# Kernel tuning notes

Hardware: AMD Instinct MI355X
Metric: run time of the kernel (lower is better)

## Reference

```python
import jax, jax.numpy as jnp
import numpy as np

D_MODEL = 1024
NUM_HEADS = 16
D_K = D_MODEL // NUM_HEADS
LN_EPS = 1e-5


def setup_inputs() -> dict:
    key = jax.random.key(0)
    ks = jax.random.split(key, 16)
    B, SQ, SK = 2, 2048, 2048
    s = 1.0 / np.sqrt(D_MODEL)
    inp = {
        "query": jax.random.normal(ks[0], (B, SQ, D_MODEL), jnp.float32),
        "key": jax.random.normal(ks[1], (B, SK, D_MODEL), jnp.float32),
        "value": jax.random.normal(ks[2], (B, SK, D_MODEL), jnp.float32),
        "mask": jax.random.randint(ks[3], (B, SQ, SK), 0, 2, jnp.int32),
        "w_q": jax.random.normal(ks[4], (D_MODEL, D_MODEL), jnp.float32) * s,
        "b_q": jnp.zeros((D_MODEL,), jnp.float32),
        "w_k": jax.random.normal(ks[5], (D_MODEL, D_MODEL), jnp.float32) * s,
        "b_k": jnp.zeros((D_MODEL,), jnp.float32),
        "w_v": jax.random.normal(ks[6], (D_MODEL, D_MODEL), jnp.float32) * s,
        "b_v": jnp.zeros((D_MODEL,), jnp.float32),
        "w_o": jax.random.normal(ks[7], (D_MODEL, D_MODEL), jnp.float32) * s,
        "b_o": jnp.zeros((D_MODEL,), jnp.float32),
        "ln_gamma": jnp.ones((D_MODEL,), jnp.float32),
        "ln_beta": jnp.zeros((D_MODEL,), jnp.float32),
    }
    return inp


def _split_heads(x):
    B, S, _ = x.shape
    return x.reshape(B, S, NUM_HEADS, D_K).transpose(0, 2, 1, 3)  # [B,H,S,Dk]


def reference(query, key, value, mask, w_q, b_q, w_k, b_k, w_v, b_v, w_o, b_o, ln_gamma, ln_beta):
    residual = query
    # torch Linear: y = x @ W.T + b
    Q = _split_heads(jnp.einsum('bsd,ed->bse', query, w_q) + b_q)
    K = _split_heads(jnp.einsum('bsd,ed->bse', key, w_k) + b_k)
    V = _split_heads(jnp.einsum('bsd,ed->bse', value, w_v) + b_v)
    scores = jnp.einsum('bhqd,bhkd->bhqk', Q, K) / jnp.sqrt(jnp.float32(D_K))
    scores = jnp.where(mask[:, None, :, :] == 0, jnp.float32(-1e9), scores)
    attn = jax.nn.softmax(scores, axis=-1)
    # dropout: eval mode (identity)
    ctx = jnp.einsum('bhqk,bhkd->bhqd', attn, V)
    B, H, SQ, Dk = ctx.shape
    ctx = ctx.transpose(0, 2, 1, 3).reshape(B, SQ, D_MODEL)
    out = jnp.einsum('bsd,ed->bse', ctx, w_o) + b_o + residual
    mu = jnp.mean(out, axis=-1, keepdims=True)
    var = jnp.mean(jnp.square(out - mu), axis=-1, keepdims=True)
    out = (out - mu) * jax.lax.rsqrt(var + LN_EPS) * ln_gamma + ln_beta
    return out
```

## Files before the change

### kernel.cpp

```cpp
#include <hip/hip_runtime.h>

typedef unsigned short u16;
typedef __attribute__((ext_vector_type(8))) short bf16x8;
typedef __attribute__((ext_vector_type(4))) float f32x4;

#define LOG2E 1.4426950408889634f
#define QSCALE (LOG2E / 8.0f)

__device__ __forceinline__ u16 f2bf(float f) {
  union { float f; unsigned u; } v; v.f = f;
  unsigned r = v.u + 0x7fffu + ((v.u >> 16) & 1u);
  return (u16)(r >> 16);
}

__device__ __forceinline__ float bf2f(u16 u) {
  union { unsigned u; float f; } v; v.u = (unsigned)u << 16; return v.f;
}

__device__ __forceinline__ void gload_lds16(const void* g, void* l) {
  __builtin_amdgcn_global_load_lds(
      (const __attribute__((address_space(1))) unsigned int*)(unsigned long long)g,
      (__attribute__((address_space(3))) unsigned int*)(unsigned int)(unsigned long long)l,
      16, 0, 0);
}

__global__ __launch_bounds__(256) void prep_kernel(
    const float* __restrict__ q, const float* __restrict__ k, const float* __restrict__ v,
    const float* __restrict__ wq, const float* __restrict__ wk, const float* __restrict__ wv,
    const float* __restrict__ wo, const int* __restrict__ mask,
    u16* __restrict__ Xq, u16* __restrict__ Xk, u16* __restrict__ Xv,
    u16* __restrict__ Wq, u16* __restrict__ Wk, u16* __restrict__ Wv, u16* __restrict__ Wo,
    unsigned long long* __restrict__ Mp) {
  const int bx = blockIdx.x;
  if (bx < 16384) {
    const float* src; u16* dst; float sc; int idx;
    if (bx < 12288) {
      int seg = bx >> 12;
      idx = (bx & 4095) * 256 + threadIdx.x;
      src = seg == 0 ? q : (seg == 1 ? k : v);
      dst = seg == 0 ? Xq : (seg == 1 ? Xk : Xv);
      sc = 1.f;
    } else {
      int t = bx - 12288, seg = t >> 10;
      idx = (t & 1023) * 256 + threadIdx.x;
      src = seg == 0 ? wq : (seg == 1 ? wk : (seg == 2 ? wv : wo));
      dst = seg == 0 ? Wq : (seg == 1 ? Wk : (seg == 2 ? Wv : Wo));
      sc = seg == 0 ? QSCALE : 1.f;
    }
    float4 x = ((const float4*)src)[idx];
    ushort4 o;
    o.x = f2bf(x.x * sc); o.y = f2bf(x.y * sc);
    o.z = f2bf(x.z * sc); o.w = f2bf(x.w * sc);
    ((ushort4*)dst)[idx] = o;
  } else {
    int gw = (((bx - 16384) * 256) + threadIdx.x) >> 6;
    int lane = threadIdx.x & 63;
    for (int w = gw; w < 131072; w += 16384) {
      int m = mask[(size_t)w * 64 + lane];
      unsigned long long b = __ballot(m != 0);
      if (lane == 0) Mp[w] = b;
    }
  }
}

__global__ __launch_bounds__(256, 3) void gemm_kernel(
    const u16* __restrict__ Xq, const u16* __restrict__ Xk, const u16* __restrict__ Xv,
    const u16* __restrict__ Wq, const u16* __restrict__ Wk, const u16* __restrict__ Wv,
    const u16* __restrict__ Wo, const u16* __restrict__ Ctx,
    const float* __restrict__ bq, const float* __restrict__ bk, const float* __restrict__ bv,
    u16* __restrict__ Qd, u16* __restrict__ Kd, u16* __restrict__ Vtd, u16* __restrict__ outp,
    int mode_base) {
  __shared__ __align__(16) u16 SH[17408];
  u16* As = SH;
  u16* Bs = SH + 4096;
  const int mode = mode_base + blockIdx.z;
  const int tid = threadIdx.x;
  const int wid = tid >> 6, l = tid & 63, quad = l >> 4, ln = l & 15;
  const int wm = wid >> 1, wn = wid & 1;

  const u16 *A, *B; const float* bias;
  if (mode == 0)      { A = Wq; B = Xq;  bias = bq; }
  else if (mode == 1) { A = Wk; B = Xk;  bias = bk; }
  else if (mode == 2) { A = Xv; B = Wv;  bias = bv; }
  else                { A = Wo; B = Ctx; bias = bq; }
  int mBase, nBase;
  if (mode == 2) { mBase = blockIdx.x * 128; nBase = blockIdx.y * 128; }
  else           { mBase = blockIdx.y * 128; nBase = blockIdx.x * 128; }

  const int koff = (mode >= 3) ? (mode - 3) * 512 : 0;
  const int kLen = (mode >= 3) ? 512 : 1024;
  const u16* Ag = A + (size_t)mBase * 1024 + koff;
  const u16* Bg = B + (size_t)nBase * 1024 + koff;

  f32x4 acc[4][4] = {};

  for (int k0 = 0; k0 < kLen; k0 += 32) {
    if (k0) __syncthreads();
    {
      int i0 = tid, i1 = tid + 256;
      gload_lds16(Ag + (size_t)(i0 & 127) * 1024 + k0 + (i0 >> 7) * 8, &As[i0 * 8]);
      gload_lds16(Ag + (size_t)(i1 & 127) * 1024 + k0 + (i1 >> 7) * 8, &As[i1 * 8]);
      gload_lds16(Bg + (size_t)(i0 & 127) * 1024 + k0 + (i0 >> 7) * 8, &Bs[i0 * 8]);
      gload_lds16(Bg + (size_t)(i1 & 127) * 1024 + k0 + (i1 >> 7) * 8, &Bs[i1 * 8]);
    }
    __syncthreads();
    bf16x8 af[4], bf[4];
#pragma unroll
    for (int i = 0; i < 4; ++i)
      af[i] = *(const bf16x8*)&As[(quad * 128 + wm * 64 + i * 16 + ln) * 8];
#pragma unroll
    for (int j = 0; j < 4; ++j)
      bf[j] = *(const bf16x8*)&Bs[(quad * 128 + wn * 64 + j * 16 + ln) * 8];
#pragma unroll
    for (int i = 0; i < 4; ++i)
#pragma unroll
      for (int j = 0; j < 4; ++j)
        acc[i][j] = __builtin_amdgcn_mfma_f32_16x16x32_bf16(af[i], bf[j], acc[i][j], 0, 0, 0);
  }

  __syncthreads();

  if (mode <= 1) {
    const float bscale = (mode == 0) ? QSCALE : 1.0f;
#pragma unroll
    for (int i = 0; i < 4; ++i) {
      int f0 = wm * 64 + i * 16 + quad * 4;
      float4 bb = *(const float4*)(bias + mBase + f0);
#pragma unroll
      for (int j = 0; j < 4; ++j) {
        int sl = wn * 64 + j * 16 + ln;
        f32x4 v = acc[i][j];
        ushort4 o;
        o.x = f2bf(v[0] + bb.x * bscale); o.y = f2bf(v[1] + bb.y * bscale);
        o.z = f2bf(v[2] + bb.z * bscale); o.w = f2bf(v[3] + bb.w * bscale);
        *(ushort4*)&SH[sl * 136 + f0] = o;
      }
    }
    __syncthreads();
    u16* dstQK = (mode == 0) ? Qd : Kd;
#pragma unroll
    for (int p = 0; p < 8; ++p) {
      int sl = p * 16 + (tid >> 4);
      int fl = (tid & 15) * 8;
      uint4 w = *(const uint4*)&SH[sl * 136 + fl];
      int s = nBase + sl, f = mBase + fl;
      int h = f >> 6, d = f & 63, b = s >> 11, sr = s & 2047;
      *(uint4*)(dstQK + (((size_t)(b * 16 + h) * 2048 + sr) * 64 + d)) = w;
    }
  } else if (mode == 2) {
#pragma unroll
    for (int j = 0; j < 4; ++j) {
      int fl = wn * 64 + j * 16 + ln;
      float bb = bias[nBase + fl];
#pragma unroll
      for (int i = 0; i < 4; ++i) {
        int s0 = wm * 64 + i * 16 + quad * 4;
        f32x4 v = acc[i][j];
        ushort4 o;
        o.x = f2bf(v[0] + bb); o.y = f2bf(v[1] + bb);
        o.z = f2bf(v[2] + bb); o.w = f2bf(v[3] + bb);
        *(ushort4*)&SH[fl * 136 + s0] = o;
      }
    }
    __syncthreads();
#pragma unroll
    for (int p = 0; p < 8; ++p) {
      int fl = p * 16 + (tid >> 4);
      int sl = (tid & 15) * 8;
      uint4 w = *(const uint4*)&SH[fl * 136 + sl];
      int f = nBase + fl, s = mBase + sl;
      int h = f >> 6, d = f & 63, b = s >> 11, sr = s & 2047;
      *(uint4*)(Vtd + (((size_t)(b * 16 + h) * 64 + d) * 2048 + sr)) = w;
    }
  } else {
    u16* dst = outp + (size_t)(mode - 3) * (4096u * 1024u);
#pragma unroll
    for (int i = 0; i < 4; ++i) {
      int f0 = wm * 64 + i * 16 + quad * 4;
#pragma unroll
      for (int j = 0; j < 4; ++j) {
        int sl = wn * 64 + j * 16 + ln;
        f32x4 v = acc[i][j];
        ushort4 o;
        o.x = f2bf(v[0]); o.y = f2bf(v[1]);
        o.z = f2bf(v[2]); o.w = f2bf(v[3]);
        *(ushort4*)&SH[sl * 136 + f0] = o;
      }
    }
    __syncthreads();
#pragma unroll
    for (int p = 0; p < 8; ++p) {
      int sl = p * 16 + (tid >> 4);
      int fl = (tid & 15) * 8;
      uint4 w = *(const uint4*)&SH[sl * 136 + fl];
      *(uint4*)(dst + (size_t)(nBase + sl) * 1024 + mBase + fl) = w;
    }
  }
}

__global__ __launch_bounds__(512, 4) void attn_kernel(
    const u16* __restrict__ Qg, const u16* __restrict__ Kg, const u16* __restrict__ Vtg,
    const unsigned* __restrict__ Mp, u16* __restrict__ ctx) {
  __shared__ __align__(16) u16 Ks0[8192];
  __shared__ __align__(16) u16 Ks1[8192];
  __shared__ __align__(16) u16 Vs0[8192];
  __shared__ __align__(16) u16 Vs1[8192];
  __shared__ __align__(16) u16 Ps[8192];
  const int tid = threadIdx.x;
  const int wid = tid >> 6, l = tid & 63, quad = l >> 4, ln = l & 15;
  const int q4 = quad * 4;
  const int L = blockIdx.x;
  const int bh = (L & 7) + 8 * (L >> 7);
  const int b = bh >> 4, h = bh & 15;
  const int qBase = ((L >> 3) & 15) * 128;
  const int wq = wid * 16;
  const int sw = (ln & 7) << 3;

  bf16x8 qf[2];
#pragma unroll
  for (int kc = 0; kc < 2; ++kc)
    qf[kc] = *(const bf16x8*)(Qg + (((size_t)bh * 2048 + qBase + wq + ln) * 64 +
                                    kc * 32 + quad * 8));

  f32x4 oacc[4] = {};
  f32x4 lsum = {};
  const bf16x8 vone = {(short)0x3F80, (short)0x3F80, (short)0x3F80, (short)0x3F80,
                       (short)0x3F80, (short)0x3F80, (short)0x3F80, (short)0x3F80};

  const unsigned* mrow = Mp + ((size_t)b * 2048 + qBase + wq + ln) * 64;

  const u16* KgB = Kg + (size_t)bh * 2048 * 64;
  const u16* VgB = Vtg + (size_t)bh * 64 * 2048;

#define STAGE_TILE(KS, VS, t_)                                                  \
  do {                                                                          \
    const int kvB_ = (t_) * 128;                                                \
    _Pragma("unroll")                                                           \
    for (int r_ = 0; r_ < 2; ++r_) {                                            \
      int c_ = r_ * 512 + tid;                                                  \
      gload_lds16(KgB + (size_t)(kvB_ + (c_ & 127)) * 64 + (c_ >> 7) * 8,       \
                  &KS[c_ * 8]);                                                 \
      gload_lds16(VgB + (size_t)(c_ & 63) * 2048 + kvB_ + (c_ >> 6) * 8,        \
                  &VS[c_ * 8]);                                                 \
    }                                                                           \
  } while (0)

#define COMPUTE_TILE(KS, VS, it_)                                                         \
  do {                                                                                    \
    unsigned ww[4];                                                                       \
    {                                                                                     \
      uint4 m0 = *(const uint4*)(mrow + (it_) * 4);                                       \
      ww[0] = m0.x; ww[1] = m0.y; ww[2] = m0.z; ww[3] = m0.w;                             \
    }                                                                                     \
    _Pragma("unroll")                                                                     \
    for (int hf = 0; hf < 2; ++hf) {                                                      \
      f32x4 s[4];                                                                         \
      __builtin_amdgcn_s_setprio(1);                                                      \
      _Pragma("unroll")                                                                   \
      for (int m2 = 0; m2 < 4; ++m2) {                                                    \
        int mt = hf * 4 + m2;                                                             \
        bf16x8 k0 = *(const bf16x8*)&KS[((0 + quad) * 128 + mt * 16 + ln) * 8];           \
        bf16x8 k1 = *(const bf16x8*)&KS[((4 + quad) * 128 + mt * 16 + ln) * 8];           \
        f32x4 z = {0.f, 0.f, 0.f, 0.f};                                                   \
        z = __builtin_amdgcn_mfma_f32_16x16x32_bf16(k0, qf[0], z, 0, 0, 0);               \
        s[m2] = __builtin_amdgcn_mfma_f32_16x16x32_bf16(k1, qf[1], z, 0, 0, 0);           \
      }                                                                                   \
      __builtin_amdgcn_s_setprio(0);                                                      \
      uint2 pk[4];                                                                        \
      _Pragma("unroll")                                                                   \
      for (int m2 = 0; m2 < 4; ++m2) {                                                    \
        int mt = hf * 4 + m2;                                                             \
        unsigned nib = (ww[mt >> 1] >> ((mt & 1) * 16 + q4)) & 0xFu;                      \
        float p0 = __builtin_amdgcn_exp2f((nib & 1u) ? s[m2][0] : -1e30f);                \
        float p1 = __builtin_amdgcn_exp2f((nib & 2u) ? s[m2][1] : -1e30f);                \
        float p2 = __builtin_amdgcn_exp2f((nib & 4u) ? s[m2][2] : -1e30f);                \
        float p3 = __builtin_amdgcn_exp2f((nib & 8u) ? s[m2][3] : -1e30f);                \
        pk[m2].x = __builtin_amdgcn_perm(__float_as_uint(p1), __float_as_uint(p0),        \
                                         0x07060302u);                                    \
        pk[m2].y = __builtin_amdgcn_perm(__float_as_uint(p3), __float_as_uint(p2),        \
                                         0x07060302u);                                    \
      }                                                                                   \
              \
      _Pragma("unroll")                                                                   \
      for (int m2 = 0; m2 < 4; ++m2)                                                      \
        *(uint2*)&Ps[(((wq + ln) * 64) + m2 * 16 + q4) ^ sw] = pk[m2];                    \
      __builtin_amdgcn_s_setprio(1);                                                      \
      _Pragma("unroll")                                                                   \
      for (int k2 = 0; k2 < 2; ++k2) {                                                    \
        int kc2 = hf * 2 + k2;                                                            \
        bf16x8 aP = *(const bf16x8*)&Ps[(((wq + ln) * 64) + k2 * 32 + quad * 8) ^ sw];    \
        _Pragma("unroll")                                                                 \
        for (int nt = 0; nt < 4; ++nt) {                                                  \
          bf16x8 bV = *(const bf16x8*)&VS[((kc2 * 4 + quad) * 64 + nt * 16 + ln) * 8];    \
          oacc[nt] = __builtin_amdgcn_mfma_f32_16x16x32_bf16(aP, bV, oacc[nt], 0, 0, 0);  \
        }                                                                                 \
        lsum = __builtin_amdgcn_mfma_f32_16x16x32_bf16(aP, vone, lsum, 0, 0, 0);          \
      }                                                                                   \
      __builtin_amdgcn_s_setprio(0);                                                      \
    }                                                                                     \
  } while (0)

  STAGE_TILE(Ks0, Vs0, 0);
#pragma unroll 1
  for (int it2 = 0; it2 < 8; ++it2) {
    __syncthreads();
    STAGE_TILE(Ks1, Vs1, 2 * it2 + 1);
    COMPUTE_TILE(Ks0, Vs0, 2 * it2);
    __syncthreads();
    if (it2 < 7) STAGE_TILE(Ks0, Vs0, 2 * it2 + 2);
    COMPUTE_TILE(Ks1, Vs1, 2 * it2 + 1);
  }
#undef STAGE_TILE
#undef COMPUTE_TILE

  __syncthreads();
#pragma unroll
  for (int r = 0; r < 4; ++r) {
    float il = 1.0f / lsum[r];
    int q = wq + q4 + r;
#pragma unroll
    for (int nt = 0; nt < 4; ++nt)
      Ps[q * 64 + nt * 16 + ln] = f2bf(oacc[nt][r] * il);
  }
  __syncthreads();
#pragma unroll
  for (int r = 0; r < 2; ++r) {
    int c = r * 512 + tid;
    int q = c >> 3, ch = c & 7;
    *(uint4*)(ctx + ((size_t)(b * 2048 + qBase + q) * 1024 + h * 64 + ch * 8)) =
        *(const uint4*)&Ps[q * 64 + ch * 8];
  }
}

__global__ __launch_bounds__(256) void ln_kernel(const u16* __restrict__ xp,
                                                 const float* __restrict__ resid,
                                                 const float* __restrict__ bo,
                                                 const float* __restrict__ gamma,
                                                 const float* __restrict__ beta,
                                                 float* __restrict__ out) {
  __shared__ float red[8];
  const int tid = threadIdx.x;
  const size_t row = blockIdx.x;
  ushort4 pa = ((const ushort4*)(xp + row * 1024))[tid];
  ushort4 pb = ((const ushort4*)(xp + 4096u * 1024u + row * 1024))[tid];
  const float4 rr = ((const float4*)(resid + row * 1024))[tid];
  const float4 bb = ((const float4*)bo)[tid];
  float4 v;
  v.x = bf2f(pa.x) + bf2f(pb.x) + rr.x + bb.x;
  v.y = bf2f(pa.y) + bf2f(pb.y) + rr.y + bb.y;
  v.z = bf2f(pa.z) + bf2f(pb.z) + rr.z + bb.z;
  v.w = bf2f(pa.w) + bf2f(pb.w) + rr.w + bb.w;
  float s1 = v.x + v.y + v.z + v.w;
  float s2 = v.x * v.x + v.y * v.y + v.z * v.z + v.w * v.w;
#pragma unroll
  for (int o = 32; o >= 1; o >>= 1) {
    s1 += __shfl_xor(s1, o);
    s2 += __shfl_xor(s2, o);
  }
  if ((tid & 63) == 0) { red[(tid >> 6) * 2] = s1; red[(tid >> 6) * 2 + 1] = s2; }
  __syncthreads();
  s1 = red[0] + red[2] + red[4] + red[6];
  s2 = red[1] + red[3] + red[5] + red[7];
  float mu = s1 * (1.f / 1024.f);
  float var = s2 * (1.f / 1024.f) - mu * mu;
  float inv = rsqrtf(var + 1e-5f);
  float4 g = ((const float4*)gamma)[tid];
  float4 be = ((const float4*)beta)[tid];
  float4 o;
  o.x = (v.x - mu) * inv * g.x + be.x;
  o.y = (v.y - mu) * inv * g.y + be.y;
  o.z = (v.z - mu) * inv * g.z + be.z;
  o.w = (v.w - mu) * inv * g.w + be.w;
  ((float4*)(out + row * 1024))[tid] = o;
}

extern "C" void kernel_launch(void* const* d_in, const int* in_sizes, int n_in,
                              void* d_out, int out_size, void* d_ws, size_t ws_size,
                              hipStream_t stream) {
  const float* query = (const float*)d_in[0];
  const float* key   = (const float*)d_in[1];
  const float* value = (const float*)d_in[2];
  const int*   mask  = (const int*)d_in[3];
  const float* w_q = (const float*)d_in[4];
  const float* b_q = (const float*)d_in[5];
  const float* w_k = (const float*)d_in[6];
  const float* b_k = (const float*)d_in[7];
  const float* w_v = (const float*)d_in[8];
  const float* b_v = (const float*)d_in[9];
  const float* w_o = (const float*)d_in[10];
  const float* b_o = (const float*)d_in[11];
  const float* ln_g = (const float*)d_in[12];
  const float* ln_b = (const float*)d_in[13];
  float* out = (float*)d_out;

  char* ws = (char*)d_ws;
  u16* Xq = (u16*)(ws + ((size_t)0 << 20));
  u16* Xk = (u16*)(ws + ((size_t)8 << 20));
  u16* Xv = (u16*)(ws + ((size_t)16 << 20));
  u16* outpre = (u16*)(ws + ((size_t)8 << 20));
  u16* Wq = (u16*)(ws + ((size_t)24 << 20));
  u16* Wk = (u16*)(ws + ((size_t)26 << 20));
  u16* Wv = (u16*)(ws + ((size_t)28 << 20));
  u16* Wo = (u16*)(ws + ((size_t)30 << 20));
  u16* Qd = (u16*)(ws + ((size_t)32 << 20));
  u16* Kd = (u16*)(ws + ((size_t)40 << 20));
  u16* Vtd = (u16*)(ws + ((size_t)48 << 20));
  unsigned long long* Mp = (unsigned long long*)(ws + ((size_t)56 << 20));
  u16* ctx = Xq;

  prep_kernel<<<20480, 256, 0, stream>>>(query, key, value, w_q, w_k, w_v, w_o, mask,
                                         Xq, Xk, Xv, Wq, Wk, Wv, Wo, Mp);
  gemm_kernel<<<dim3(32, 8, 3), 256, 0, stream>>>(Xq, Xk, Xv, Wq, Wk, Wv, Wo, ctx,
      b_q, b_k, b_v, Qd, Kd, Vtd, outpre, 0);
  attn_kernel<<<dim3(512), 512, 0, stream>>>(Qd, Kd, Vtd, (const unsigned*)Mp, ctx);
  gemm_kernel<<<dim3(32, 8, 2), 256, 0, stream>>>(Xq, Xk, Xv, Wq, Wk, Wv, Wo, ctx,
      b_q, b_k, b_v, Qd, Kd, Vtd, outpre, 3);
  ln_kernel<<<4096, 256, 0, stream>>>(outpre, query, b_o, ln_g, ln_b, out);
}
```

Measured before the change: 297.1 us.

## Split attention KV tile across 4 wave groups with 1024-thread blocks and LDS reduction

The attention kernel moves from 512 to 1024 threads per block. Each wave now handles 32 query rows against a quarter of every 128-key tile, rather than 16 rows against the whole tile. Partial output and row-sum accumulators from the four key groups are reduced serially through shared memory at the end. The aim is more waves in flight to hide latency and more reuse of K/V fragments across two query tiles. In exchange it adds a serialized reduction with extra syncs, an unpadded P buffer with a different layout, and possible occupancy limits from the 1024-thread blocks.

```diff
diff --git a/kernel.cpp b/kernel.cpp
--- a/kernel.cpp
+++ b/kernel.cpp
@@ -198,36 +198,41 @@
   }
 }
 
-__global__ __launch_bounds__(512, 4) void attn_kernel(
+__global__ __launch_bounds__(1024, 4) void attn_kernel(
     const u16* __restrict__ Qg, const u16* __restrict__ Kg, const u16* __restrict__ Vtg,
     const unsigned* __restrict__ Mp, u16* __restrict__ ctx) {
   __shared__ __align__(16) u16 Ks0[8192];
   __shared__ __align__(16) u16 Ks1[8192];
   __shared__ __align__(16) u16 Vs0[8192];
   __shared__ __align__(16) u16 Vs1[8192];
-  __shared__ __align__(16) u16 Ps[8192];
+  __shared__ __align__(16) u16 Pall[4 * 128 * 40];
   const int tid = threadIdx.x;
   const int wid = tid >> 6, l = tid & 63, quad = l >> 4, ln = l & 15;
   const int q4 = quad * 4;
+  const int qb = wid >> 2, g = wid & 3;
+  const int wq = qb * 32;
   const int L = blockIdx.x;
   const int bh = (L & 7) + 8 * (L >> 7);
   const int b = bh >> 4, h = bh & 15;
   const int qBase = ((L >> 3) & 15) * 128;
-  const int wq = wid * 16;
-  const int sw = (ln & 7) << 3;
-
-  bf16x8 qf[2];
-#pragma unroll
-  for (int kc = 0; kc < 2; ++kc)
-    qf[kc] = *(const bf16x8*)(Qg + (((size_t)bh * 2048 + qBase + wq + ln) * 64 +
-                                    kc * 32 + quad * 8));
-
-  f32x4 oacc[4] = {};
-  f32x4 lsum = {};
+  u16* Ps = &Pall[g * 128 * 40];
+
+  bf16x8 qf[2][2];
+#pragma unroll
+  for (int qt = 0; qt < 2; ++qt)
+#pragma unroll
+    for (int kc = 0; kc < 2; ++kc)
+      qf[qt][kc] = *(const bf16x8*)(Qg + (((size_t)bh * 2048 + qBase + wq + qt * 16 + ln) * 64 +
+                                          kc * 32 + quad * 8));
+
+  f32x4 oacc[2][4] = {};
+  f32x4 lsum[2] = {};
   const bf16x8 vone = {(short)0x3F80, (short)0x3F80, (short)0x3F80, (short)0x3F80,
                        (short)0x3F80, (short)0x3F80, (short)0x3F80, (short)0x3F80};
 
-  const unsigned* mrow = Mp + ((size_t)b * 2048 + qBase + wq + ln) * 64;
+  const unsigned* mrow[2];
+  mrow[0] = Mp + ((size_t)b * 2048 + qBase + wq + ln) * 64;
+  mrow[1] = mrow[0] + 16 * 64;
 
   const u16* KgB = Kg + (size_t)bh * 2048 * 64;
   const u16* VgB = Vtg + (size_t)bh * 64 * 2048;
@@ -235,69 +240,63 @@
 #define STAGE_TILE(KS, VS, t_)                                                  \
   do {                                                                          \
     const int kvB_ = (t_) * 128;                                                \
-    _Pragma("unroll")                                                           \
-    for (int r_ = 0; r_ < 2; ++r_) {                                            \
-      int c_ = r_ * 512 + tid;                                                  \
-      gload_lds16(KgB + (size_t)(kvB_ + (c_ & 127)) * 64 + (c_ >> 7) * 8,       \
-                  &KS[c_ * 8]);                                                 \
-      gload_lds16(VgB + (size_t)(c_ & 63) * 2048 + kvB_ + (c_ >> 6) * 8,        \
-                  &VS[c_ * 8]);                                                 \
-    }                                                                           \
+    gload_lds16(KgB + (size_t)(kvB_ + (tid & 127)) * 64 + (tid >> 7) * 8,       \
+                &KS[tid * 8]);                                                  \
+    gload_lds16(VgB + (size_t)(tid & 63) * 2048 + kvB_ + (tid >> 6) * 8,        \
+                &VS[tid * 8]);                                                  \
   } while (0)
 
 #define COMPUTE_TILE(KS, VS, it_)                                                         \
   do {                                                                                    \
-    unsigned ww[4];                                                                       \
-    {                                                                                     \
-      uint4 m0 = *(const uint4*)(mrow + (it_) * 4);                                       \
-      ww[0] = m0.x; ww[1] = m0.y; ww[2] = m0.z; ww[3] = m0.w;                             \
+    unsigned mw[2];                                                                       \
+    mw[0] = mrow[0][(it_) * 4 + g];                                                       \
+    mw[1] = mrow[1][(it_) * 4 + g];                                                       \
+    f32x4 s[2][2];                                                                        \
+    __builtin_amdgcn_s_setprio(1);                                                        \
+    _Pragma("unroll")                                                                     \
+    for (int mtl = 0; mtl < 2; ++mtl) {                                                   \
+      int mt = g * 2 + mtl;                                                               \
+      bf16x8 k0 = *(const bf16x8*)&KS[((0 + quad) * 128 + mt * 16 + ln) * 8];             \
+      bf16x8 k1 = *(const bf16x8*)&KS[((4 + quad) * 128 + mt * 16 + ln) * 8];             \
+      _Pragma("unroll")                                                                   \
+      for (int qt = 0; qt < 2; ++qt) {                                                    \
+        f32x4 z = {0.f, 0.f, 0.f, 0.f};                                                   \
+        z = __builtin_amdgcn_mfma_f32_16x16x32_bf16(k0, qf[qt][0], z, 0, 0, 0);           \
+        s[mtl][qt] = __builtin_amdgcn_mfma_f32_16x16x32_bf16(k1, qf[qt][1], z, 0, 0, 0);  \
+      }                                                                                   \
     }                                                                                     \
+    __builtin_amdgcn_s_setprio(0);                                                        \
     _Pragma("unroll")                                                                     \
-    for (int hf = 0; hf < 2; ++hf) {                                                      \
-      f32x4 s[4];                                                                         \
-      __builtin_amdgcn_s_setprio(1);                                                      \
+    for (int qt = 0; qt < 2; ++qt) {                                                      \
+      int qrow = wq + qt * 16 + ln;                                                       \
       _Pragma("unroll")                                                                   \
-      for (int m2 = 0; m2 < 4; ++m2) {                                                    \
-        int mt = hf * 4 + m2;                                                             \
-        bf16x8 k0 = *(const bf16x8*)&KS[((0 + quad) * 128 + mt * 16 + ln) * 8];           \
-        bf16x8 k1 = *(const bf16x8*)&KS[((4 + quad) * 128 + mt * 16 + ln) * 8];           \
-        f32x4 z = {0.f, 0.f, 0.f, 0.f};                                                   \
-        z = __builtin_amdgcn_mfma_f32_16x16x32_bf16(k0, qf[0], z, 0, 0, 0);               \
-        s[m2] = __builtin_amdgcn_mfma_f32_16x16x32_bf16(k1, qf[1], z, 0, 0, 0);           \
+      for (int mtl = 0; mtl < 2; ++mtl) {                                                 \
+        unsigned nib = (mw[qt] >> (mtl * 16 + q4)) & 0xFu;                                \
+        float p0 = __builtin_amdgcn_exp2f((nib & 1u) ? s[mtl][qt][0] : -1e30f);           \
+        float p1 = __builtin_amdgcn_exp2f((nib & 2u) ? s[mtl][qt][1] : -1e30f);           \
+        float p2 = __builtin_amdgcn_exp2f((nib & 4u) ? s[mtl][qt][2] : -1e30f);           \
+        float p3 = __builtin_amdgcn_exp2f((nib & 8u) ? s[mtl][qt][3] : -1e30f);           \
+        uint2 pk;                                                                         \
+        pk.x = __builtin_amdgcn_perm(__float_as_uint(p1), __float_as_uint(p0),            \
+                                     0x07060302u);                                        \
+        pk.y = __builtin_amdgcn_perm(__float_as_uint(p3), __float_as_uint(p2),            \
+                                     0x07060302u);                                        \
+        *(uint2*)&Ps[qrow * 40 + mtl * 16 + q4] = pk;                                     \
       }                                                                                   \
-      __builtin_amdgcn_s_setprio(0);                                                      \
-      uint2 pk[4];                                                                        \
+    }                                                                                     \
+               \
+    __builtin_amdgcn_s_setprio(1);                                                        \
+    _Pragma("unroll")                                                                     \
+    for (int qt = 0; qt < 2; ++qt) {                                                      \
+      bf16x8 aP = *(const bf16x8*)&Ps[(wq + qt * 16 + ln) * 40 + quad * 8];               \
       _Pragma("unroll")                                                                   \
-      for (int m2 = 0; m2 < 4; ++m2) {                                                    \
-        int mt = hf * 4 + m2;                                                             \
-        unsigned nib = (ww[mt >> 1] >> ((mt & 1) * 16 + q4)) & 0xFu;                      \
-        float p0 = __builtin_amdgcn_exp2f((nib & 1u) ? s[m2][0] : -1e30f);                \
-        float p1 = __builtin_amdgcn_exp2f((nib & 2u) ? s[m2][1] : -1e30f);                \
-        float p2 = __builtin_amdgcn_exp2f((nib & 4u) ? s[m2][2] : -1e30f);                \
-        float p3 = __builtin_amdgcn_exp2f((nib & 8u) ? s[m2][3] : -1e30f);                \
-        pk[m2].x = __builtin_amdgcn_perm(__float_as_uint(p1), __float_as_uint(p0),        \
-                                         0x07060302u);                                    \
-        pk[m2].y = __builtin_amdgcn_perm(__float_as_uint(p3), __float_as_uint(p2),        \
-                                         0x07060302u);                                    \
+      for (int nt = 0; nt < 4; ++nt) {                                                    \
+        bf16x8 bV = *(const bf16x8*)&VS[((g * 4 + quad) * 64 + nt * 16 + ln) * 8];        \
+        oacc[qt][nt] = __builtin_amdgcn_mfma_f32_16x16x32_bf16(aP, bV, oacc[qt][nt], 0, 0, 0); \
       }                                                                                   \
-              \
-      _Pragma("unroll")                                                                   \
-      for (int m2 = 0; m2 < 4; ++m2)                                                      \
-        *(uint2*)&Ps[(((wq + ln) * 64) + m2 * 16 + q4) ^ sw] = pk[m2];                    \
-      __builtin_amdgcn_s_setprio(1);                                                      \
-      _Pragma("unroll")                                                                   \
-      for (int k2 = 0; k2 < 2; ++k2) {                                                    \
-        int kc2 = hf * 2 + k2;                                                            \
-        bf16x8 aP = *(const bf16x8*)&Ps[(((wq + ln) * 64) + k2 * 32 + quad * 8) ^ sw];    \
-        _Pragma("unroll")                                                                 \
-        for (int nt = 0; nt < 4; ++nt) {                                                  \
-          bf16x8 bV = *(const bf16x8*)&VS[((kc2 * 4 + quad) * 64 + nt * 16 + ln) * 8];    \
-          oacc[nt] = __builtin_amdgcn_mfma_f32_16x16x32_bf16(aP, bV, oacc[nt], 0, 0, 0);  \
-        }                                                                                 \
-        lsum = __builtin_amdgcn_mfma_f32_16x16x32_bf16(aP, vone, lsum, 0, 0, 0);          \
-      }                                                                                   \
-      __builtin_amdgcn_s_setprio(0);                                                      \
+      lsum[qt] = __builtin_amdgcn_mfma_f32_16x16x32_bf16(aP, vone, lsum[qt], 0, 0, 0);    \
     }                                                                                     \
+    __builtin_amdgcn_s_setprio(0);                                                        \
   } while (0)
 
   STAGE_TILE(Ks0, Vs0, 0);
@@ -314,21 +313,38 @@
 #undef COMPUTE_TILE
 
   __syncthreads();
-#pragma unroll
-  for (int r = 0; r < 4; ++r) {
-    float il = 1.0f / lsum[r];
-    int q = wq + q4 + r;
-#pragma unroll
-    for (int nt = 0; nt < 4; ++nt)
-      Ps[q * 64 + nt * 16 + ln] = f2bf(oacc[nt][r] * il);
-  }
-  __syncthreads();
-#pragma unroll
-  for (int r = 0; r < 2; ++r) {
-    int c = r * 512 + tid;
-    int q = c >> 3, ch = c & 7;
-    *(uint4*)(ctx + ((size_t)(b * 2048 + qBase + q) * 1024 + h * 64 + ch * 8)) =
-        *(const uint4*)&Ps[q * 64 + ch * 8];
+  float* OS = (float*)Pall;
+#pragma unroll 1
+  for (int gg = 0; gg < 4; ++gg) {
+    if (g == gg) {
+#pragma unroll
+      for (int qt = 0; qt < 2; ++qt)
+#pragma unroll
+        for (int r = 0; r < 4; ++r) {
+          int qr = wq + qt * 16 + q4 + r;
+#pragma unroll
+          for (int nt = 0; nt < 4; ++nt) {
+            int col = nt * 16 + ln;
+            if (gg == 0) OS[qr * 66 + col] = oacc[qt][nt][r];
+            else         OS[qr * 66 + col] += oacc[qt][nt][r];
+          }
+          if (ln == 0) {
+            if (gg == 0) OS[qr * 66 + 64] = lsum[qt][r];
+            else         OS[qr * 66 + 64] += lsum[qt][r];
+          }
+        }
+    }
+    __syncthreads();
+  }
+
+  {
+    int qr = tid >> 3, ch = tid & 7;
+    float il = 1.0f / OS[qr * 66 + 64];
+    union { u16 us[8]; uint4 u4; } o;
+#pragma unroll
+    for (int j = 0; j < 8; ++j)
+      o.us[j] = f2bf(OS[qr * 66 + ch * 8 + j] * il);
+    *(uint4*)(ctx + ((size_t)(b * 2048 + qBase + qr) * 1024 + h * 64 + ch * 8)) = o.u4;
   }
 }
 
@@ -412,7 +428,7 @@
                                          Xq, Xk, Xv, Wq, Wk, Wv, Wo, Mp);
   gemm_kernel<<<dim3(32, 8, 3), 256, 0, stream>>>(Xq, Xk, Xv, Wq, Wk, Wv, Wo, ctx,
       b_q, b_k, b_v, Qd, Kd, Vtd, outpre, 0);
-  attn_kernel<<<dim3(512), 512, 0, stream>>>(Qd, Kd, Vtd, (const unsigned*)Mp, ctx);
+  attn_kernel<<<dim3(512), 1024, 0, stream>>>(Qd, Kd, Vtd, (const unsigned*)Mp, ctx);
   gemm_kernel<<<dim3(32, 8, 2), 256, 0, stream>>>(Xq, Xk, Xv, Wq, Wk, Wv, Wo, ctx,
       b_q, b_k, b_v, Qd, Kd, Vtd, outpre, 3);
   ln_kernel<<<4096, 256, 0, stream>>>(outpre, query, b_o, ln_g, ln_b, out);
```

New measurement: 339.1 us. 1.14x slower.

## Double-buffer LDS tiles in projection GEMM k-loop

Applied to the files above, without the earlier changes.

Splits the shared-memory A/B tiles into two buffers and restructures the GEMM k-loop so the global-to-LDS load of the next k-slice is issued before the MFMA compute on the current slice. This is meant to hide global load latency behind matrix math instead of serialising load, barrier, compute on every step. It reuses LDS already allocated for the epilogue, so occupancy is unchanged. The loop is unrolled by two, which assumes kLen is a multiple of 64.

```diff
diff --git a/kernel.cpp b/kernel.cpp
--- a/kernel.cpp
+++ b/kernel.cpp
@@ -71,8 +71,10 @@
     u16* __restrict__ Qd, u16* __restrict__ Kd, u16* __restrict__ Vtd, u16* __restrict__ outp,
     int mode_base) {
   __shared__ __align__(16) u16 SH[17408];
-  u16* As = SH;
-  u16* Bs = SH + 4096;
+  u16* As0 = SH;
+  u16* Bs0 = SH + 4096;
+  u16* As1 = SH + 8192;
+  u16* Bs1 = SH + 12288;
   const int mode = mode_base + blockIdx.z;
   const int tid = threadIdx.x;
   const int wid = tid >> 6, l = tid & 63, quad = l >> 4, ln = l & 15;
@@ -94,29 +96,45 @@
 
   f32x4 acc[4][4] = {};
 
-  for (int k0 = 0; k0 < kLen; k0 += 32) {
-    if (k0) __syncthreads();
-    {
-      int i0 = tid, i1 = tid + 256;
-      gload_lds16(Ag + (size_t)(i0 & 127) * 1024 + k0 + (i0 >> 7) * 8, &As[i0 * 8]);
-      gload_lds16(Ag + (size_t)(i1 & 127) * 1024 + k0 + (i1 >> 7) * 8, &As[i1 * 8]);
-      gload_lds16(Bg + (size_t)(i0 & 127) * 1024 + k0 + (i0 >> 7) * 8, &Bs[i0 * 8]);
-      gload_lds16(Bg + (size_t)(i1 & 127) * 1024 + k0 + (i1 >> 7) * 8, &Bs[i1 * 8]);
-    }
-    __syncthreads();
-    bf16x8 af[4], bf[4];
-#pragma unroll
-    for (int i = 0; i < 4; ++i)
-      af[i] = *(const bf16x8*)&As[(quad * 128 + wm * 64 + i * 16 + ln) * 8];
-#pragma unroll
-    for (int j = 0; j < 4; ++j)
-      bf[j] = *(const bf16x8*)&Bs[(quad * 128 + wn * 64 + j * 16 + ln) * 8];
-#pragma unroll
-    for (int i = 0; i < 4; ++i)
-#pragma unroll
-      for (int j = 0; j < 4; ++j)
-        acc[i][j] = __builtin_amdgcn_mfma_f32_16x16x32_bf16(af[i], bf[j], acc[i][j], 0, 0, 0);
-  }
+#define GSTAGE(AS, BS, t_)                                                      \
+  do {                                                                          \
+    const int k0_ = (t_) * 32;                                                  \
+    int i0 = tid, i1 = tid + 256;                                               \
+    gload_lds16(Ag + (size_t)(i0 & 127) * 1024 + k0_ + (i0 >> 7) * 8, &AS[i0 * 8]); \
+    gload_lds16(Ag + (size_t)(i1 & 127) * 1024 + k0_ + (i1 >> 7) * 8, &AS[i1 * 8]); \
+    gload_lds16(Bg + (size_t)(i0 & 127) * 1024 + k0_ + (i0 >> 7) * 8, &BS[i0 * 8]); \
+    gload_lds16(Bg + (size_t)(i1 & 127) * 1024 + k0_ + (i1 >> 7) * 8, &BS[i1 * 8]); \
+  } while (0)
+
+#define GCOMP(AS, BS)                                                           \
+  do {                                                                          \
+    bf16x8 af[4], bf[4];                                                        \
+    _Pragma("unroll")                                                           \
+    for (int i = 0; i < 4; ++i)                                                 \
+      af[i] = *(const bf16x8*)&AS[(quad * 128 + wm * 64 + i * 16 + ln) * 8];    \
+    _Pragma("unroll")                                                           \
+    for (int j = 0; j < 4; ++j)                                                 \
+      bf[j] = *(const bf16x8*)&BS[(quad * 128 + wn * 64 + j * 16 + ln) * 8];    \
+    _Pragma("unroll")                                                           \
+    for (int i = 0; i < 4; ++i)                                                 \
+      _Pragma("unroll")                                                         \
+      for (int j = 0; j < 4; ++j)                                               \
+        acc[i][j] = __builtin_amdgcn_mfma_f32_16x16x32_bf16(af[i], bf[j], acc[i][j], 0, 0, 0); \
+  } while (0)
+
+  const int nt2 = kLen >> 6;
+  GSTAGE(As0, Bs0, 0);
+#pragma unroll 1
+  for (int it2 = 0; it2 < nt2; ++it2) {
+    __syncthreads();
+    GSTAGE(As1, Bs1, 2 * it2 + 1);
+    GCOMP(As0, Bs0);
+    __syncthreads();
+    if (it2 < nt2 - 1) GSTAGE(As0, Bs0, 2 * it2 + 2);
+    GCOMP(As1, Bs1);
+  }
+#undef GSTAGE
+#undef GCOMP
 
   __syncthreads();
 
```

New measurement: 295.0 us. About the same (-0.7%).
